# Kernel optimization log

Hardware: AMD Instinct MI355X
Metric: run time of the kernel (lower is better)

Reference implementation:

```python
import jax, jax.numpy as jnp
import numpy as np

N_ING, N_DIR = 100000, 50000
E = 1000000
H, D = 4, 16          # heads, per-head dim
HID = H * D           # 64
LAT, COND = 32, 8
F_ING, F_DIR = 16, 8
OUT_ING = 16


def _han_edge(x_src, x_dst, att_s, att_d, edge_index, n_dst):
    # HANConv per-edge-type attention message passing.
    src, dst = edge_index[0], edge_index[1]
    a = jax.nn.leaky_relu(
        jnp.einsum('nhd,hd->nh', x_src, att_s)[src]
        + jnp.einsum('nhd,hd->nh', x_dst, att_d)[dst],
        negative_slope=0.2)                               # [E, H]
    amax = jax.ops.segment_max(a, dst, num_segments=n_dst)
    ex = jnp.exp(a - amax[dst])
    denom = jax.ops.segment_sum(ex, dst, num_segments=n_dst)
    alpha = ex / (denom[dst] + 1e-16)                     # PyG softmax eps
    out = jax.ops.segment_sum(x_src[src] * alpha[:, :, None], dst,
                              num_segments=n_dst)         # [n_dst, H, D]
    return jax.nn.relu(out.reshape(n_dst, HID))


def _group(outs, q, Wk, bk):
    # HANConv semantic-level attention across edge types.
    s = jnp.stack(outs)                                   # [T, N, HID]
    score = jnp.tanh(s @ Wk + bk).mean(axis=1) @ q        # [T]
    attn = jax.nn.softmax(score)
    return jnp.einsum('t,tnf->nf', attn, s)


def setup_inputs() -> dict:
    key = jax.random.key(0)
    ks = jax.random.split(key, 32)
    def ei(k, n_src, n_dst):
        k1, k2 = jax.random.split(k)
        return jnp.stack([jax.random.randint(k1, (E,), 0, n_src),
                          jax.random.randint(k2, (E,), 0, n_dst)]).astype(jnp.int64)
    s = 0.1
    inp = {
        'x_ing': jax.random.normal(ks[0], (N_ING, F_ING), jnp.float32),
        'x_dir': jax.random.normal(ks[1], (N_DIR, F_DIR), jnp.float32),
        'cond':  jax.random.normal(ks[2], (COND,), jnp.float32),
        'eps':   jax.random.normal(ks[3], (1, LAT), jnp.float32),
        'ei_cooc':     ei(ks[4], N_ING, N_DIR),
        'ei_used':     ei(ks[5], N_ING, N_DIR),
        'ei_contains': ei(ks[6], N_DIR, N_ING),
        'ei_pairs':    ei(ks[7], N_DIR, N_DIR),
        'ei_follows':  ei(ks[8], N_DIR, N_DIR),
        # node-type projections
        'W_pi': jax.random.normal(ks[9],  (F_ING, HID)) * s,
        'b_pi': jnp.zeros((HID,)),
        'W_pd': jax.random.normal(ks[10], (F_DIR, HID)) * s,
        'b_pd': jnp.zeros((HID,)),
        # semantic attention
        'Wk': jax.random.normal(ks[21], (HID, HID)) * s,
        'bk': jnp.zeros((HID,)),
        'q':  jax.random.normal(ks[22], (HID,)) * s,
        # VAE heads (input: 2*HID + COND)
        'W_mu': jax.random.normal(ks[23], (2 * HID + COND, LAT)) * s,
        'b_mu': jnp.zeros((LAT,)),
        'W_lv': jax.random.normal(ks[24], (2 * HID + COND, LAT)) * s,
        'b_lv': jnp.zeros((LAT,)),
        # decoder (fc1 is dead code in the original forward)
        'W_fc3': jax.random.normal(ks[25], (LAT, HID)) * s,
        'b_fc3': jnp.zeros((HID,)),
        'W_fc2': jax.random.normal(ks[26], (HID, OUT_ING)) * s,
        'b_fc2': jnp.zeros((OUT_ING,)),
    }
    for i, name in enumerate(['cooc', 'used', 'contains', 'pairs', 'follows']):
        inp[f'as_{name}'] = jax.random.normal(ks[11 + i], (H, D)) * s
        inp[f'ad_{name}'] = jax.random.normal(ks[16 + i], (H, D)) * s
    return inp


def reference(x_ing, x_dir, cond, eps,
              ei_cooc, ei_used, ei_contains, ei_pairs, ei_follows,
              W_pi, b_pi, W_pd, b_pd,
              as_cooc, ad_cooc, as_used, ad_used, as_contains, ad_contains,
              as_pairs, ad_pairs, as_follows, ad_follows,
              Wk, bk, q, W_mu, b_mu, W_lv, b_lv,
              W_fc3, b_fc3, W_fc2, b_fc2):
    # node-type projections -> [N, H, D]
    h_ing = (x_ing @ W_pi + b_pi).reshape(N_ING, H, D)
    h_dir = (x_dir @ W_pd + b_pd).reshape(N_DIR, H, D)

    o_cooc = _han_edge(h_ing, h_dir, as_cooc, ad_cooc, ei_cooc, N_DIR)
    o_used = _han_edge(h_ing, h_dir, as_used, ad_used, ei_used, N_DIR)
    o_cont = _han_edge(h_dir, h_ing, as_contains, ad_contains, ei_contains, N_ING)
    o_pair = _han_edge(h_dir, h_dir, as_pairs, ad_pairs, ei_pairs, N_DIR)
    o_foll = _han_edge(h_dir, h_dir, as_follows, ad_follows, ei_follows, N_DIR)

    out_ing = _group([o_cont], q, Wk, bk)                       # [N_ING, HID]
    out_dir = _group([o_cooc, o_used, o_pair, o_foll], q, Wk, bk)

    ingre_pool = out_ing.mean(axis=0, keepdims=True)            # [1, HID]
    direc_pool = out_dir.mean(axis=0, keepdims=True)
    graph_repr = jnp.concatenate([ingre_pool, direc_pool, cond[None]], axis=1)

    mu = graph_repr @ W_mu + b_mu
    logvar = graph_repr @ W_lv + b_lv
    z = mu + eps * jnp.exp(0.5 * logvar)

    # decoder: fc1 branch is overwritten in the original; effective path below
    recon = jnp.tanh(jax.nn.relu(z @ W_fc3 + b_fc3) @ W_fc2 + b_fc2)  # [1, OUT_ING]
    return recon, mu, logvar
```

## Files before the change

### kernel.cpp

```cpp
#include <hip/hip_runtime.h>
#include <math.h>

#define N_ING 100000
#define N_DIR 50000
#define NE    1000000
#define NDST_TOTAL 300000
#define NBUCK 4688
#define BA    64
#define NBLK_A (5 * BA)
#define I4PT  (NE / 4)
#define PB_ING 192
#define PB_DIR 96

typedef float v2f __attribute__((ext_vector_type(2)));

__global__ __launch_bounds__(256) void k1_kernel(
    const int* __restrict__ e0, const int* __restrict__ e1,
    const int* __restrict__ e2, const int* __restrict__ e3,
    const int* __restrict__ e4, int* __restrict__ blockcnt,
    const float* __restrict__ x_ing, const float* __restrict__ W_pi,
    const float* __restrict__ b_pi,
    const float* __restrict__ as_cooc, const float* __restrict__ as_used,
    const float* __restrict__ ad_contains,
    unsigned* __restrict__ h8_ing, float* __restrict__ s_ing,
    const float* __restrict__ x_dir, const float* __restrict__ W_pd,
    const float* __restrict__ b_pd,
    const float* __restrict__ ad_cooc, const float* __restrict__ ad_used,
    const float* __restrict__ as_contains, const float* __restrict__ as_pairs,
    const float* __restrict__ ad_pairs, const float* __restrict__ as_follows,
    const float* __restrict__ ad_follows,
    unsigned* __restrict__ h8_dir, float* __restrict__ s_dir)
{
    __shared__ int hist[NBUCK];
    __shared__ float sW[16 * 64];
    __shared__ float sbb[64];
    __shared__ float satt[7 * 64];
    __shared__ float sx[4][16];
    __shared__ float srow[4][64];

    const int bid = blockIdx.x;
    const int tid = threadIdx.x;
    if (bid < NBLK_A) {
        const int type = bid >> 6, blk = bid & 63;
        const int* ei = type == 0 ? e0 : type == 1 ? e1 : type == 2 ? e2
                      : type == 3 ? e3 : e4;
        const int base = type == 0 ? 0 : type == 1 ? 50000 : type == 2 ? 100000
                       : type == 3 ? 200000 : 250000;
        for (int i = tid; i < NBUCK; i += 256) hist[i] = 0;
        __syncthreads();
        const int4* d4 = (const int4*)(ei + NE);
        for (int i = blk * 256 + tid; i < I4PT; i += BA * 256) {
            int4 d = d4[i];
            atomicAdd(&hist[(base + d.x) >> 6], 1);
            atomicAdd(&hist[(base + d.y) >> 6], 1);
            atomicAdd(&hist[(base + d.z) >> 6], 1);
            atomicAdd(&hist[(base + d.w) >> 6], 1);
        }
        __syncthreads();
        int* row = blockcnt + (size_t)bid * NBUCK;
        for (int i = tid; i < NBUCK; i += 256) row[i] = hist[i];
    } else if (bid < NBLK_A + PB_ING) {
        const int g = tid >> 6, t = tid & 63;
        for (int i = tid; i < 16 * 64; i += 256) sW[i] = W_pi[i];
        if (tid < 64) {
            sbb[tid] = b_pi[tid];
            satt[tid]       = as_cooc[tid];
            satt[64 + tid]  = as_used[tid];
            satt[128 + tid] = ad_contains[tid];
        }
        __syncthreads();
        for (int q = bid - NBLK_A; q < N_ING / 4; q += PB_ING) {
            int n = q * 4 + g;
            if (t < 16) sx[g][t] = x_ing[(size_t)n * 16 + t];
            __syncthreads();
            float s = sbb[t];
#pragma unroll
            for (int i = 0; i < 16; ++i) s += sx[g][i] * sW[i * 64 + t];
            srow[g][t] = s;
            __syncthreads();
            if (t < 16) {
                int w0 = __builtin_amdgcn_cvt_pk_fp8_f32(srow[g][t * 4], srow[g][t * 4 + 1], 0, false);
                int w  = __builtin_amdgcn_cvt_pk_fp8_f32(srow[g][t * 4 + 2], srow[g][t * 4 + 3], w0, true);
                h8_ing[(size_t)n * 16 + t] = (unsigned)w;
            }
            if (t < 12) {
                int slot = t >> 2, hh = t & 3;
                float sc = 0.f;
#pragma unroll
                for (int d = 0; d < 16; ++d)
                    sc += srow[g][hh * 16 + d] * satt[slot * 64 + hh * 16 + d];
                s_ing[(size_t)n * 12 + t] = sc;
            }
            __syncthreads();
        }
    } else {
        const int g = tid >> 6, t = tid & 63;
        for (int i = tid; i < 8 * 64; i += 256) sW[i] = W_pd[i];
        if (tid < 64) {
            sbb[tid] = b_pd[tid];
            satt[tid]        = ad_cooc[tid];
            satt[64  + tid]  = ad_used[tid];
            satt[128 + tid]  = as_contains[tid];
            satt[192 + tid]  = as_pairs[tid];
            satt[256 + tid]  = ad_pairs[tid];
            satt[320 + tid]  = as_follows[tid];
            satt[384 + tid]  = ad_follows[tid];
        }
        __syncthreads();
        for (int q = bid - NBLK_A - PB_ING; q < N_DIR / 4; q += PB_DIR) {
            int n = q * 4 + g;
            if (t < 8) sx[g][t] = x_dir[(size_t)n * 8 + t];
            __syncthreads();
            float s = sbb[t];
#pragma unroll
            for (int i = 0; i < 8; ++i) s += sx[g][i] * sW[i * 64 + t];
            srow[g][t] = s;
            __syncthreads();
            if (t < 16) {
                int w0 = __builtin_amdgcn_cvt_pk_fp8_f32(srow[g][t * 4], srow[g][t * 4 + 1], 0, false);
                int w  = __builtin_amdgcn_cvt_pk_fp8_f32(srow[g][t * 4 + 2], srow[g][t * 4 + 3], w0, true);
                h8_dir[(size_t)n * 16 + t] = (unsigned)w;
            }
            if (t < 28) {
                int slot = t >> 2, hh = t & 3;
                float sc = 0.f;
#pragma unroll
                for (int d = 0; d < 16; ++d)
                    sc += srow[g][hh * 16 + d] * satt[slot * 64 + hh * 16 + d];
                s_dir[(size_t)n * 28 + t] = sc;
            }
            __syncthreads();
        }
    }
}

__global__ __launch_bounds__(256) void k2_kernel(
    const int* __restrict__ blockcnt, int* __restrict__ blockbase,
    int* __restrict__ bbase, int* __restrict__ btot, int* __restrict__ cursor)
{
    __shared__ int sh[256];
    __shared__ int bw;
    int b = blockIdx.x * 256 + threadIdx.x;
    bool act = b < NBUCK;
    int tot = 0;
    if (act)
        for (int k = 0; k < NBLK_A; ++k) tot += blockcnt[(size_t)k * NBUCK + b];
    sh[threadIdx.x] = tot;
    __syncthreads();
    for (int off = 1; off < 256; off <<= 1) {
        int v = (threadIdx.x >= off) ? sh[threadIdx.x - off] : 0;
        __syncthreads();
        sh[threadIdx.x] += v;
        __syncthreads();
    }
    if (threadIdx.x == 255) bw = atomicAdd(cursor, sh[255]);
    __syncthreads();
    if (act) {
        int base = bw + sh[threadIdx.x] - tot;
        bbase[b] = base;
        btot[b] = tot;
        int run = base;
        for (int k = 0; k < NBLK_A; ++k) {
            int c = blockcnt[(size_t)k * NBUCK + b];
            blockbase[(size_t)k * NBUCK + b] = run;
            run += c;
        }
    }
}

__global__ __launch_bounds__(256) void k3_kernel(
    const int* __restrict__ e0, const int* __restrict__ e1,
    const int* __restrict__ e2, const int* __restrict__ e3,
    const int* __restrict__ e4, const int* __restrict__ blockbase,
    int2* __restrict__ bpair)
{
    __shared__ int cur[NBUCK];
    const int bid = blockIdx.x, tid = threadIdx.x;
    const int type = bid >> 6, blk = bid & 63;
    const int* ei = type == 0 ? e0 : type == 1 ? e1 : type == 2 ? e2
                  : type == 3 ? e3 : e4;
    const int base = type == 0 ? 0 : type == 1 ? 50000 : type == 2 ? 100000
                   : type == 3 ? 200000 : 250000;
    const int* row = blockbase + (size_t)bid * NBUCK;
    for (int i = tid; i < NBUCK; i += 256) cur[i] = row[i];
    __syncthreads();
    const int4* s4 = (const int4*)ei;
    const int4* d4 = (const int4*)(ei + NE);
    for (int i = blk * 256 + tid; i < I4PT; i += BA * 256) {
        int4 s = s4[i];
        int4 d = d4[i];
        int g0 = base + d.x, g1 = base + d.y, g2 = base + d.z, g3 = base + d.w;
        int p0 = atomicAdd(&cur[g0 >> 6], 1);
        int p1 = atomicAdd(&cur[g1 >> 6], 1);
        int p2 = atomicAdd(&cur[g2 >> 6], 1);
        int p3 = atomicAdd(&cur[g3 >> 6], 1);
        bpair[p0] = make_int2(s.x, g0);
        bpair[p1] = make_int2(s.y, g1);
        bpair[p2] = make_int2(s.z, g2);
        bpair[p3] = make_int2(s.w, g3);
    }
}

__global__ __launch_bounds__(256) void k4_kernel(
    const int2* __restrict__ bpair, const int* __restrict__ bbase,
    const int* __restrict__ btot, int* __restrict__ perm,
    int* __restrict__ start, int* __restrict__ cnt)
{
    __shared__ int h[64], sc[64], cu[64];
    const int b = blockIdx.x, tid = threadIdx.x;
    const int jb = bbase[b], n = btot[b];
    if (tid < 64) h[tid] = 0;
    __syncthreads();
    for (int i = tid; i < n; i += 256)
        atomicAdd(&h[bpair[jb + i].y & 63], 1);
    __syncthreads();
    if (tid == 0) {
        int r = 0;
        for (int i = 0; i < 64; ++i) { sc[i] = r; cu[i] = r; r += h[i]; }
    }
    __syncthreads();
    if (tid < 64) {
        int dg = b * 64 + tid;
        if (dg < NDST_TOTAL) {
            start[dg] = jb + sc[tid];
            cnt[dg] = h[tid];
        }
    }
    for (int i = tid; i < n; i += 256) {
        int2 p = bpair[jb + i];
        int pos = atomicAdd(&cu[p.y & 63], 1);
        perm[jb + pos] = p.x;
    }
}

__global__ __launch_bounds__(256) void agg_all_kernel(
    const int* __restrict__ perm, const int* __restrict__ start,
    const int* __restrict__ cnttot,
    const unsigned* __restrict__ h8_ing, const unsigned* __restrict__ h8_dir,
    const float* __restrict__ s_ing, const float* __restrict__ s_dir,
    const float* __restrict__ Wk, const float* __restrict__ bk,
    float* __restrict__ pool_ing, float* __restrict__ pool_dir,
    float* __restrict__ sem_dir)
{
    __shared__ float sWk[64 * 64];
    __shared__ float srow[4][64];
    __shared__ float sred[4][64];
    const int t = threadIdx.x & 63, w = threadIdx.x >> 6;
    const int g  = t >> 4;
    const int l4 = t & 15;
    const int hq = l4 >> 2;
    for (int i = threadIdx.x; i < 4096; i += 256) sWk[i] = Wk[i];
    const float bkf = bk[t];
    float p_ing = 0.f;
    float p0 = 0.f, p1 = 0.f, p2 = 0.f, p3 = 0.f;
    float m0 = 0.f, m1 = 0.f, m2 = 0.f, m3 = 0.f;
    __syncthreads();
    const int nwaves = gridDim.x * 4;
    for (int d = blockIdx.x * 4 + w; d < NDST_TOTAL; d += nwaves) {
        int type, ld;
        const float *ssrc, *sdst;
        const unsigned* hsrc;
        int ss, soff, ds, doff;
        if (d < 50000)       { type = 0; ld = d;          ssrc = s_ing; ss = 12; soff = 0;  sdst = s_dir; ds = 28; doff = 0;  hsrc = h8_ing; }
        else if (d < 100000) { type = 1; ld = d - 50000;  ssrc = s_ing; ss = 12; soff = 4;  sdst = s_dir; ds = 28; doff = 4;  hsrc = h8_ing; }
        else if (d < 200000) { type = 2; ld = d - 100000; ssrc = s_dir; ss = 28; soff = 8;  sdst = s_ing; ds = 12; doff = 8;  hsrc = h8_dir; }
        else if (d < 250000) { type = 3; ld = d - 200000; ssrc = s_dir; ss = 28; soff = 12; sdst = s_dir; ds = 28; doff = 16; hsrc = h8_dir; }
        else                 { type = 4; ld = d - 250000; ssrc = s_dir; ss = 28; soff = 20; sdst = s_dir; ds = 28; doff = 24; hsrc = h8_dir; }
        float adst = sdst[(size_t)ld * ds + doff + hq];
        int jb = start[d], je = jb + cnttot[d];
        float4 acc = make_float4(0.f, 0.f, 0.f, 0.f);
        float dsum = 0.f;
        for (int j = jb; j < je; j += 8) {
            int j0 = j + g, j1 = j + 4 + g;
            bool v0 = j0 < je, v1 = j1 < je;
            int s0 = perm[v0 ? j0 : je - 1];
            int s1 = perm[v1 ? j1 : je - 1];
            float c0 = ssrc[(size_t)s0 * ss + soff + hq];
            float c1 = ssrc[(size_t)s1 * ss + soff + hq];
            unsigned u0 = hsrc[(size_t)s0 * 16 + l4];
            unsigned u1 = hsrc[(size_t)s1 * 16 + l4];
            float a0 = c0 + adst; a0 = a0 > 0.f ? a0 : 0.2f * a0;
            float a1 = c1 + adst; a1 = a1 > 0.f ? a1 : 0.2f * a1;
            float e0 = v0 ? __expf(a0) : 0.f;
            float e1 = v1 ? __expf(a1) : 0.f;
            dsum += e0 + e1;
            v2f lo0 = __builtin_amdgcn_cvt_pk_f32_fp8((int)u0, false);
            v2f hi0 = __builtin_amdgcn_cvt_pk_f32_fp8((int)u0, true);
            v2f lo1 = __builtin_amdgcn_cvt_pk_f32_fp8((int)u1, false);
            v2f hi1 = __builtin_amdgcn_cvt_pk_f32_fp8((int)u1, true);
            acc.x += lo0.x * e0 + lo1.x * e1;
            acc.y += lo0.y * e0 + lo1.y * e1;
            acc.z += hi0.x * e0 + hi1.x * e1;
            acc.w += hi0.y * e0 + hi1.y * e1;
        }
#pragma unroll
        for (int mask = 16; mask <= 32; mask <<= 1) {
            acc.x += __shfl_xor(acc.x, mask, 64);
            acc.y += __shfl_xor(acc.y, mask, 64);
            acc.z += __shfl_xor(acc.z, mask, 64);
            acc.w += __shfl_xor(acc.w, mask, 64);
            dsum  += __shfl_xor(dsum,  mask, 64);
        }
        float inv = 1.f / (dsum + 1e-16f);
        float4 v4 = make_float4(fmaxf(acc.x * inv, 0.f), fmaxf(acc.y * inv, 0.f),
                                fmaxf(acc.z * inv, 0.f), fmaxf(acc.w * inv, 0.f));
        if (g == 0) *(float4*)&srow[w][l4 * 4] = v4;
        float v = srow[w][t];
        if (type == 2) {
            p_ing += v;
        } else {
            float a2 = bkf;
#pragma unroll
            for (int k = 0; k < 64; ++k) a2 += srow[w][k] * sWk[k * 64 + t];
            float tv = tanhf(a2);
            if (type == 0)      { p0 += v; m0 += tv; }
            else if (type == 1) { p1 += v; m1 += tv; }
            else if (type == 3) { p2 += v; m2 += tv; }
            else                { p3 += v; m3 += tv; }
        }
    }
    float vals[9] = { p_ing, p0, p1, p2, p3, m0, m1, m2, m3 };
    float* outs[9] = { pool_ing, pool_dir, pool_dir + 64, pool_dir + 128,
                       pool_dir + 192, sem_dir, sem_dir + 64, sem_dir + 128,
                       sem_dir + 192 };
    for (int i = 0; i < 9; ++i) {
        __syncthreads();
        sred[w][t] = vals[i];
        __syncthreads();
        if (w == 0)
            atomicAdd(&outs[i][t], sred[0][t] + sred[1][t] + sred[2][t] + sred[3][t]);
    }
}

__global__ __launch_bounds__(64) void final_kernel(
    const float* __restrict__ pool_ing, const float* __restrict__ pool_dir,
    const float* __restrict__ sem_dir, const float* __restrict__ q,
    const float* __restrict__ cond, const float* __restrict__ eps,
    const float* __restrict__ W_mu, const float* __restrict__ b_mu,
    const float* __restrict__ W_lv, const float* __restrict__ b_lv,
    const float* __restrict__ W_fc3, const float* __restrict__ b_fc3,
    const float* __restrict__ W_fc2, const float* __restrict__ b_fc2,
    float* __restrict__ out)
{
    __shared__ float gr[136];
    __shared__ float sc[4], attn[4];
    __shared__ float z[32], hfc[64];
    int t = threadIdx.x;
    if (t < 4) {
        float s = 0.f;
        for (int f = 0; f < 64; ++f)
            s += (sem_dir[t * 64 + f] / (float)N_DIR) * q[f];
        sc[t] = s;
    }
    gr[t] = pool_ing[t] / (float)N_ING;
    __syncthreads();
    if (t == 0) {
        float m = fmaxf(fmaxf(sc[0], sc[1]), fmaxf(sc[2], sc[3]));
        float ssum = 0.f;
        for (int i = 0; i < 4; ++i) { attn[i] = expf(sc[i] - m); ssum += attn[i]; }
        for (int i = 0; i < 4; ++i) attn[i] /= ssum;
    }
    __syncthreads();
    {
        float v = 0.f;
        for (int tt = 0; tt < 4; ++tt)
            v += attn[tt] * (pool_dir[tt * 64 + t] / (float)N_DIR);
        gr[64 + t] = v;
    }
    if (t < 8) gr[128 + t] = cond[t];
    __syncthreads();
    if (t < 32) {
        float m = b_mu[t], lv = b_lv[t];
        for (int i = 0; i < 136; ++i) {
            float g = gr[i];
            m  += g * W_mu[i * 32 + t];
            lv += g * W_lv[i * 32 + t];
        }
        out[16 + t] = m;
        out[48 + t] = lv;
        z[t] = m + eps[t] * expf(0.5f * lv);
    }
    __syncthreads();
    {
        float v = b_fc3[t];
        for (int j = 0; j < 32; ++j) v += z[j] * W_fc3[j * 64 + t];
        hfc[t] = fmaxf(v, 0.f);
    }
    __syncthreads();
    if (t < 16) {
        float v = b_fc2[t];
        for (int f = 0; f < 64; ++f) v += hfc[f] * W_fc2[f * 16 + t];
        out[t] = tanhf(v);
    }
}

extern "C" void kernel_launch(void* const* d_in, const int* in_sizes, int n_in,
                              void* d_out, int out_size, void* d_ws, size_t ws_size,
                              hipStream_t stream) {
    const float* x_ing = (const float*)d_in[0];
    const float* x_dir = (const float*)d_in[1];
    const float* cond  = (const float*)d_in[2];
    const float* eps   = (const float*)d_in[3];
    const int* ei_cooc     = (const int*)d_in[4];
    const int* ei_used     = (const int*)d_in[5];
    const int* ei_contains = (const int*)d_in[6];
    const int* ei_pairs    = (const int*)d_in[7];
    const int* ei_follows  = (const int*)d_in[8];
    const float* W_pi = (const float*)d_in[9];
    const float* b_pi = (const float*)d_in[10];
    const float* W_pd = (const float*)d_in[11];
    const float* b_pd = (const float*)d_in[12];
    const float* Wk   = (const float*)d_in[13];
    const float* bk   = (const float*)d_in[14];
    const float* q    = (const float*)d_in[15];
    const float* W_mu = (const float*)d_in[16];
    const float* b_mu = (const float*)d_in[17];
    const float* W_lv = (const float*)d_in[18];
    const float* b_lv = (const float*)d_in[19];
    const float* W_fc3 = (const float*)d_in[20];
    const float* b_fc3 = (const float*)d_in[21];
    const float* W_fc2 = (const float*)d_in[22];
    const float* b_fc2 = (const float*)d_in[23];
    const float* as_cooc     = (const float*)d_in[24];
    const float* ad_cooc     = (const float*)d_in[25];
    const float* as_used     = (const float*)d_in[26];
    const float* ad_used     = (const float*)d_in[27];
    const float* as_contains = (const float*)d_in[28];
    const float* ad_contains = (const float*)d_in[29];
    const float* as_pairs    = (const float*)d_in[30];
    const float* ad_pairs    = (const float*)d_in[31];
    const float* as_follows  = (const float*)d_in[32];
    const float* ad_follows  = (const float*)d_in[33];

    int2* bpair = (int2*)d_ws;
    unsigned* h8_ing = (unsigned*)(bpair + (size_t)5 * NE);
    unsigned* h8_dir = h8_ing + (size_t)N_ING * 16;
    float* s_ing = (float*)(h8_dir + (size_t)N_DIR * 16);
    float* s_dir = s_ing + (size_t)N_ING * 12;
    int*   perm   = (int*)(s_dir + (size_t)N_DIR * 28);
    int*   blockcnt  = perm + (size_t)5 * NE;
    int*   blockbase = blockcnt + (size_t)NBLK_A * NBUCK;
    int*   bbase  = blockbase + (size_t)NBLK_A * NBUCK;
    int*   btot   = bbase + NBUCK;
    int*   start  = btot + NBUCK;
    int*   cnt    = start + NDST_TOTAL;
    int*   cursor = cnt + NDST_TOTAL;
    float* pool_ing = (float*)(cursor + 1);
    float* pool_dir = pool_ing + 64;
    float* sem_dir  = pool_dir + 256;

    hipMemsetAsync(cursor, 0, (1 + 64 + 256 + 256) * sizeof(int), stream);

    k1_kernel<<<NBLK_A + PB_ING + PB_DIR, 256, 0, stream>>>(
        ei_cooc, ei_used, ei_contains, ei_pairs, ei_follows, blockcnt,
        x_ing, W_pi, b_pi, as_cooc, as_used, ad_contains, h8_ing, s_ing,
        x_dir, W_pd, b_pd, ad_cooc, ad_used, as_contains, as_pairs, ad_pairs,
        as_follows, ad_follows, h8_dir, s_dir);

    k2_kernel<<<(NBUCK + 255) / 256, 256, 0, stream>>>(
        blockcnt, blockbase, bbase, btot, cursor);

    k3_kernel<<<NBLK_A, 256, 0, stream>>>(
        ei_cooc, ei_used, ei_contains, ei_pairs, ei_follows, blockbase, bpair);

    k4_kernel<<<NBUCK, 256, 0, stream>>>(bpair, bbase, btot, perm, start, cnt);

    agg_all_kernel<<<2048, 256, 0, stream>>>(
        perm, start, cnt, h8_ing, h8_dir, s_ing, s_dir, Wk, bk,
        pool_ing, pool_dir, sem_dir);

    final_kernel<<<1, 64, 0, stream>>>(
        pool_ing, pool_dir, sem_dir, q, cond, eps,
        W_mu, b_mu, W_lv, b_lv, W_fc3, b_fc3, W_fc2, b_fc2, (float*)d_out);
}
```

Before: 568.0 us.

## Pack bucket pairs into 32 bits, store scores as fp16, shrink partition blocks

```diff
diff --git a/kernel.cpp b/kernel.cpp
--- a/kernel.cpp
+++ b/kernel.cpp
@@ -1,4 +1,5 @@
 #include <hip/hip_runtime.h>
+#include <hip/hip_fp16.h>
 #include <math.h>
 
 #define N_ING 100000
@@ -6,15 +7,15 @@
 #define NE    1000000
 #define NDST_TOTAL 300000
 #define NBUCK 4688
-#define BA    64
-#define NBLK_A (5 * BA)
+#define BA    16
+#define NBK   (5 * BA)
 #define I4PT  (NE / 4)
-#define PB_ING 192
-#define PB_DIR 96
+#define PB_ING 384
+#define PB_DIR 192
 
 typedef float v2f __attribute__((ext_vector_type(2)));
 
-__global__ __launch_bounds__(256) void k1_kernel(
+__global__ __launch_bounds__(256) void kA_kernel(
     const int* __restrict__ e0, const int* __restrict__ e1,
     const int* __restrict__ e2, const int* __restrict__ e3,
     const int* __restrict__ e4, int* __restrict__ blockcnt,
@@ -22,14 +23,14 @@
     const float* __restrict__ b_pi,
     const float* __restrict__ as_cooc, const float* __restrict__ as_used,
     const float* __restrict__ ad_contains,
-    unsigned* __restrict__ h8_ing, float* __restrict__ s_ing,
+    unsigned* __restrict__ h8_ing, __half* __restrict__ s_ing,
     const float* __restrict__ x_dir, const float* __restrict__ W_pd,
     const float* __restrict__ b_pd,
     const float* __restrict__ ad_cooc, const float* __restrict__ ad_used,
     const float* __restrict__ as_contains, const float* __restrict__ as_pairs,
     const float* __restrict__ ad_pairs, const float* __restrict__ as_follows,
     const float* __restrict__ ad_follows,
-    unsigned* __restrict__ h8_dir, float* __restrict__ s_dir)
+    unsigned* __restrict__ h8_dir, __half* __restrict__ s_dir)
 {
     __shared__ int hist[NBUCK];
     __shared__ float sW[16 * 64];
@@ -40,8 +41,8 @@
 
     const int bid = blockIdx.x;
     const int tid = threadIdx.x;
-    if (bid < NBLK_A) {
-        const int type = bid >> 6, blk = bid & 63;
+    if (bid < NBK) {
+        const int type = bid / BA, blk = bid % BA;
         const int* ei = type == 0 ? e0 : type == 1 ? e1 : type == 2 ? e2
                       : type == 3 ? e3 : e4;
         const int base = type == 0 ? 0 : type == 1 ? 50000 : type == 2 ? 100000
@@ -59,7 +60,7 @@
         __syncthreads();
         int* row = blockcnt + (size_t)bid * NBUCK;
         for (int i = tid; i < NBUCK; i += 256) row[i] = hist[i];
-    } else if (bid < NBLK_A + PB_ING) {
+    } else if (bid < NBK + PB_ING) {
         const int g = tid >> 6, t = tid & 63;
         for (int i = tid; i < 16 * 64; i += 256) sW[i] = W_pi[i];
         if (tid < 64) {
@@ -69,7 +70,7 @@
             satt[128 + tid] = ad_contains[tid];
         }
         __syncthreads();
-        for (int q = bid - NBLK_A; q < N_ING / 4; q += PB_ING) {
+        for (int q = bid - NBK; q < N_ING / 4; q += PB_ING) {
             int n = q * 4 + g;
             if (t < 16) sx[g][t] = x_ing[(size_t)n * 16 + t];
             __syncthreads();
@@ -89,7 +90,7 @@
 #pragma unroll
                 for (int d = 0; d < 16; ++d)
                     sc += srow[g][hh * 16 + d] * satt[slot * 64 + hh * 16 + d];
-                s_ing[(size_t)n * 12 + t] = sc;
+                s_ing[(size_t)n * 12 + t] = __float2half(sc);
             }
             __syncthreads();
         }
@@ -107,7 +108,7 @@
             satt[384 + tid]  = ad_follows[tid];
         }
         __syncthreads();
-        for (int q = bid - NBLK_A - PB_ING; q < N_DIR / 4; q += PB_DIR) {
+        for (int q = bid - NBK - PB_ING; q < N_DIR / 4; q += PB_DIR) {
             int n = q * 4 + g;
             if (t < 8) sx[g][t] = x_dir[(size_t)n * 8 + t];
             __syncthreads();
@@ -127,7 +128,7 @@
 #pragma unroll
                 for (int d = 0; d < 16; ++d)
                     sc += srow[g][hh * 16 + d] * satt[slot * 64 + hh * 16 + d];
-                s_dir[(size_t)n * 28 + t] = sc;
+                s_dir[(size_t)n * 28 + t] = __float2half(sc);
             }
             __syncthreads();
         }
@@ -138,32 +139,46 @@
     const int* __restrict__ blockcnt, int* __restrict__ blockbase,
     int* __restrict__ bbase, int* __restrict__ btot, int* __restrict__ cursor)
 {
-    __shared__ int sh[256];
+    __shared__ int part[4][64];
+    __shared__ int tots[64];
+    __shared__ int scn[64];
     __shared__ int bw;
-    int b = blockIdx.x * 256 + threadIdx.x;
-    bool act = b < NBUCK;
-    int tot = 0;
-    if (act)
-        for (int k = 0; k < NBLK_A; ++k) tot += blockcnt[(size_t)k * NBUCK + b];
-    sh[threadIdx.x] = tot;
-    __syncthreads();
-    for (int off = 1; off < 256; off <<= 1) {
-        int v = (threadIdx.x >= off) ? sh[threadIdx.x - off] : 0;
-        __syncthreads();
-        sh[threadIdx.x] += v;
-        __syncthreads();
-    }
-    if (threadIdx.x == 255) bw = atomicAdd(cursor, sh[255]);
-    __syncthreads();
-    if (act) {
-        int base = bw + sh[threadIdx.x] - tot;
-        bbase[b] = base;
-        btot[b] = tot;
-        int run = base;
-        for (int k = 0; k < NBLK_A; ++k) {
-            int c = blockcnt[(size_t)k * NBUCK + b];
+    const int tid = threadIdx.x;
+    const int kq = tid >> 6, bl = tid & 63;
+    const int b = blockIdx.x * 64 + bl;
+    const int K = NBK / 4;
+    int ps = 0;
+    if (b < NBUCK)
+        for (int k = kq * K; k < kq * K + K; ++k)
+            ps += blockcnt[(size_t)k * NBUCK + b];
+    part[kq][bl] = ps;
+    __syncthreads();
+    if (tid < 64) {
+        int t = part[0][tid] + part[1][tid] + part[2][tid] + part[3][tid];
+        tots[tid] = t;
+        scn[tid] = t;
+    }
+    __syncthreads();
+    for (int off = 1; off < 64; off <<= 1) {
+        int v = 0;
+        if (tid < 64 && tid >= off) v = scn[tid - off];
+        __syncthreads();
+        if (tid < 64) scn[tid] += v;
+        __syncthreads();
+    }
+    if (tid == 63) bw = atomicAdd(cursor, scn[63]);
+    __syncthreads();
+    if (b < NBUCK) {
+        int bs = bw + scn[bl] - tots[bl];
+        if (kq == 0) {
+            bbase[b] = bs;
+            btot[b] = tots[bl];
+        }
+        int run = bs;
+        for (int q = 0; q < kq; ++q) run += part[q][bl];
+        for (int k = kq * K; k < kq * K + K; ++k) {
             blockbase[(size_t)k * NBUCK + b] = run;
-            run += c;
+            run += blockcnt[(size_t)k * NBUCK + b];
         }
     }
 }
@@ -172,11 +187,11 @@
     const int* __restrict__ e0, const int* __restrict__ e1,
     const int* __restrict__ e2, const int* __restrict__ e3,
     const int* __restrict__ e4, const int* __restrict__ blockbase,
-    int2* __restrict__ bpair)
+    unsigned* __restrict__ bpair)
 {
     __shared__ int cur[NBUCK];
     const int bid = blockIdx.x, tid = threadIdx.x;
-    const int type = bid >> 6, blk = bid & 63;
+    const int type = bid / BA, blk = bid % BA;
     const int* ei = type == 0 ? e0 : type == 1 ? e1 : type == 2 ? e2
                   : type == 3 ? e3 : e4;
     const int base = type == 0 ? 0 : type == 1 ? 50000 : type == 2 ? 100000
@@ -194,15 +209,15 @@
         int p1 = atomicAdd(&cur[g1 >> 6], 1);
         int p2 = atomicAdd(&cur[g2 >> 6], 1);
         int p3 = atomicAdd(&cur[g3 >> 6], 1);
-        bpair[p0] = make_int2(s.x, g0);
-        bpair[p1] = make_int2(s.y, g1);
-        bpair[p2] = make_int2(s.z, g2);
-        bpair[p3] = make_int2(s.w, g3);
+        bpair[p0] = ((unsigned)(g0 & 63) << 17) | (unsigned)s.x;
+        bpair[p1] = ((unsigned)(g1 & 63) << 17) | (unsigned)s.y;
+        bpair[p2] = ((unsigned)(g2 & 63) << 17) | (unsigned)s.z;
+        bpair[p3] = ((unsigned)(g3 & 63) << 17) | (unsigned)s.w;
     }
 }
 
 __global__ __launch_bounds__(256) void k4_kernel(
-    const int2* __restrict__ bpair, const int* __restrict__ bbase,
+    const unsigned* __restrict__ bpair, const int* __restrict__ bbase,
     const int* __restrict__ btot, int* __restrict__ perm,
     int* __restrict__ start, int* __restrict__ cnt)
 {
@@ -212,7 +227,7 @@
     if (tid < 64) h[tid] = 0;
     __syncthreads();
     for (int i = tid; i < n; i += 256)
-        atomicAdd(&h[bpair[jb + i].y & 63], 1);
+        atomicAdd(&h[bpair[jb + i] >> 17], 1);
     __syncthreads();
     if (tid == 0) {
         int r = 0;
@@ -227,9 +242,9 @@
         }
     }
     for (int i = tid; i < n; i += 256) {
-        int2 p = bpair[jb + i];
-        int pos = atomicAdd(&cu[p.y & 63], 1);
-        perm[jb + pos] = p.x;
+        unsigned p = bpair[jb + i];
+        int pos = atomicAdd(&cu[p >> 17], 1);
+        perm[jb + pos] = (int)(p & 0x1FFFF);
     }
 }
 
@@ -237,7 +252,7 @@
     const int* __restrict__ perm, const int* __restrict__ start,
     const int* __restrict__ cnttot,
     const unsigned* __restrict__ h8_ing, const unsigned* __restrict__ h8_dir,
-    const float* __restrict__ s_ing, const float* __restrict__ s_dir,
+    const __half* __restrict__ s_ing, const __half* __restrict__ s_dir,
     const float* __restrict__ Wk, const float* __restrict__ bk,
     float* __restrict__ pool_ing, float* __restrict__ pool_dir,
     float* __restrict__ sem_dir)
@@ -258,7 +273,7 @@
     const int nwaves = gridDim.x * 4;
     for (int d = blockIdx.x * 4 + w; d < NDST_TOTAL; d += nwaves) {
         int type, ld;
-        const float *ssrc, *sdst;
+        const __half *ssrc, *sdst;
         const unsigned* hsrc;
         int ss, soff, ds, doff;
         if (d < 50000)       { type = 0; ld = d;          ssrc = s_ing; ss = 12; soff = 0;  sdst = s_dir; ds = 28; doff = 0;  hsrc = h8_ing; }
@@ -266,7 +281,7 @@
         else if (d < 200000) { type = 2; ld = d - 100000; ssrc = s_dir; ss = 28; soff = 8;  sdst = s_ing; ds = 12; doff = 8;  hsrc = h8_dir; }
         else if (d < 250000) { type = 3; ld = d - 200000; ssrc = s_dir; ss = 28; soff = 12; sdst = s_dir; ds = 28; doff = 16; hsrc = h8_dir; }
         else                 { type = 4; ld = d - 250000; ssrc = s_dir; ss = 28; soff = 20; sdst = s_dir; ds = 28; doff = 24; hsrc = h8_dir; }
-        float adst = sdst[(size_t)ld * ds + doff + hq];
+        float adst = __half2float(sdst[(size_t)ld * ds + doff + hq]);
         int jb = start[d], je = jb + cnttot[d];
         float4 acc = make_float4(0.f, 0.f, 0.f, 0.f);
         float dsum = 0.f;
@@ -275,8 +290,8 @@
             bool v0 = j0 < je, v1 = j1 < je;
             int s0 = perm[v0 ? j0 : je - 1];
             int s1 = perm[v1 ? j1 : je - 1];
-            float c0 = ssrc[(size_t)s0 * ss + soff + hq];
-            float c1 = ssrc[(size_t)s1 * ss + soff + hq];
+            float c0 = __half2float(ssrc[(size_t)s0 * ss + soff + hq]);
+            float c1 = __half2float(ssrc[(size_t)s1 * ss + soff + hq]);
             unsigned u0 = hsrc[(size_t)s0 * 16 + l4];
             unsigned u1 = hsrc[(size_t)s1 * 16 + l4];
             float a0 = c0 + adst; a0 = a0 > 0.f ? a0 : 0.2f * a0;
@@ -432,15 +447,15 @@
     const float* as_follows  = (const float*)d_in[32];
     const float* ad_follows  = (const float*)d_in[33];
 
-    int2* bpair = (int2*)d_ws;
-    unsigned* h8_ing = (unsigned*)(bpair + (size_t)5 * NE);
+    unsigned* bpair = (unsigned*)d_ws;
+    unsigned* h8_ing = bpair + (size_t)5 * NE;
     unsigned* h8_dir = h8_ing + (size_t)N_ING * 16;
-    float* s_ing = (float*)(h8_dir + (size_t)N_DIR * 16);
-    float* s_dir = s_ing + (size_t)N_ING * 12;
-    int*   perm   = (int*)(s_dir + (size_t)N_DIR * 28);
+    __half* s_ing = (__half*)(h8_dir + (size_t)N_DIR * 16);
+    __half* s_dir = s_ing + (size_t)N_ING * 12;
+    int*   perm  = (int*)(s_dir + (size_t)N_DIR * 28);
     int*   blockcnt  = perm + (size_t)5 * NE;
-    int*   blockbase = blockcnt + (size_t)NBLK_A * NBUCK;
-    int*   bbase  = blockbase + (size_t)NBLK_A * NBUCK;
+    int*   blockbase = blockcnt + (size_t)NBK * NBUCK;
+    int*   bbase  = blockbase + (size_t)NBK * NBUCK;
     int*   btot   = bbase + NBUCK;
     int*   start  = btot + NBUCK;
     int*   cnt    = start + NDST_TOTAL;
@@ -451,16 +466,16 @@
 
     hipMemsetAsync(cursor, 0, (1 + 64 + 256 + 256) * sizeof(int), stream);
 
-    k1_kernel<<<NBLK_A + PB_ING + PB_DIR, 256, 0, stream>>>(
+    kA_kernel<<<NBK + PB_ING + PB_DIR, 256, 0, stream>>>(
         ei_cooc, ei_used, ei_contains, ei_pairs, ei_follows, blockcnt,
         x_ing, W_pi, b_pi, as_cooc, as_used, ad_contains, h8_ing, s_ing,
         x_dir, W_pd, b_pd, ad_cooc, ad_used, as_contains, as_pairs, ad_pairs,
         as_follows, ad_follows, h8_dir, s_dir);
 
-    k2_kernel<<<(NBUCK + 255) / 256, 256, 0, stream>>>(
+    k2_kernel<<<(NBUCK + 63) / 64, 256, 0, stream>>>(
         blockcnt, blockbase, bbase, btot, cursor);
 
-    k3_kernel<<<NBLK_A, 256, 0, stream>>>(
+    k3_kernel<<<NBK, 256, 0, stream>>>(
         ei_cooc, ei_used, ei_contains, ei_pairs, ei_follows, blockbase, bpair);
 
     k4_kernel<<<NBUCK, 256, 0, stream>>>(bpair, bbase, btot, perm, start, cnt);
```

New measurement: 520.4 us, median of 2. 8.4% less time.
